# Kernel tuning notes

Hardware: AMD Instinct MI355X
Metric: run time of the kernel (lower is better)

Reference implementation:

```python
import jax, jax.numpy as jnp
import numpy as np

B, S, D, H = 2, 2048, 1024, 16
HD = D // H
DFF = 4 * D
EPS = 1e-5


def layernorm(x, g, b):
    mu = jnp.mean(x, axis=-1, keepdims=True)
    var = jnp.mean((x - mu) ** 2, axis=-1, keepdims=True)
    return (x - mu) * jax.lax.rsqrt(var + EPS) * g + b


def setup_inputs() -> dict:
    key = jax.random.key(0)
    ks = jax.random.split(key, 16)
    sc = 0.02
    return {
        "x": jax.random.normal(ks[0], (B, S, D), jnp.float32),
        "pos_emb": jax.random.normal(ks[1], (S, D), jnp.float32),
        "ln1_g": jnp.ones((D,), jnp.float32),
        "ln1_b": jnp.zeros((D,), jnp.float32),
        "w_qkv": jax.random.normal(ks[2], (D, 3 * D), jnp.float32) * sc,
        "b_qkv": jnp.zeros((3 * D,), jnp.float32),
        "w_o": jax.random.normal(ks[3], (D, D), jnp.float32) * sc,
        "b_o": jnp.zeros((D,), jnp.float32),
        "ln2_g": jnp.ones((D,), jnp.float32),
        "ln2_b": jnp.zeros((D,), jnp.float32),
        "w_fc": jax.random.normal(ks[4], (D, DFF), jnp.float32) * sc,
        "b_fc": jnp.zeros((DFF,), jnp.float32),
        "w_proj": jax.random.normal(ks[5], (DFF, D), jnp.float32) * sc,
        "b_proj": jnp.zeros((D,), jnp.float32),
    }


def reference(x, pos_emb, ln1_g, ln1_b, w_qkv, b_qkv, w_o, b_o,
              ln2_g, ln2_b, w_fc, b_fc, w_proj, b_proj):
    # --- attention sub-block: x + attn(norm1(x) + pos_emb) ---
    h = layernorm(x, ln1_g, ln1_b) + pos_emb  # [B,S,D]
    qkv = h @ w_qkv + b_qkv                    # [B,S,3D]
    qkv = qkv.reshape(B, S, 3, H, HD).transpose(2, 0, 3, 1, 4)  # [3,B,H,S,HD]
    q, k, v = qkv[0], qkv[1], qkv[2]
    # naive full attention: materialize [B,H,S,S]
    w = jnp.einsum('bhqd,bhkd->bhqk', q, k) / jnp.sqrt(jnp.float32(HD))
    causal = jnp.tril(jnp.ones((S, S), bool))  # True = keep
    w = jnp.where(causal, w, -jnp.inf)
    a = jax.nn.softmax(w, axis=-1)
    out = jnp.einsum('bhqk,bhkd->bhqd', a, v)   # [B,H,S,HD]
    out = out.transpose(0, 2, 1, 3).reshape(B, S, D)
    x = x + out @ w_o + b_o
    # --- MLP sub-block: x + mlp(norm2(x)) ---
    m = layernorm(x, ln2_g, ln2_b)
    m = jax.nn.gelu(m @ w_fc + b_fc) @ w_proj + b_proj
    return x + m
```

## Files before the change

kernel.cpp:

```cpp
#include <hip/hip_runtime.h>
#include <hip/hip_bf16.h>

typedef __hip_bfloat16 bf16_t;
typedef __bf16 bf16x8 __attribute__((ext_vector_type(8)));
typedef float f32x4 __attribute__((ext_vector_type(4)));

__device__ __forceinline__ void gload_lds16(const void* g, void* l) {
  __builtin_amdgcn_global_load_lds(
      (const __attribute__((address_space(1))) void*)g,
      (__attribute__((address_space(3))) void*)l, 16, 0, 0);
}

__device__ __forceinline__ unsigned short f2bf(float f) {
  bf16_t h = __float2bfloat16(f);
  return reinterpret_cast<unsigned short&>(h);
}

__global__ __launch_bounds__(256) void wtrans_kernel(
    const float* __restrict__ in, bf16_t* __restrict__ out, int K, int N) {
  __shared__ float tile[32][33];
  int tx = threadIdx.x, ty = threadIdx.y;
  int n = blockIdx.x * 32 + tx;
  int k0 = blockIdx.y * 32 + ty;
#pragma unroll
  for (int j = 0; j < 32; j += 8) tile[ty + j][tx] = in[(size_t)(k0 + j) * N + n];
  __syncthreads();
  int k = blockIdx.y * 32 + tx;
  int n0 = blockIdx.x * 32 + ty;
#pragma unroll
  for (int j = 0; j < 32; j += 8)
    out[(size_t)(n0 + j) * K + k] = __float2bfloat16(tile[tx][ty + j]);
}

__global__ __launch_bounds__(256) void ln_kernel(
    const float* __restrict__ x, const float* __restrict__ g,
    const float* __restrict__ b, const float* __restrict__ pos,
    bf16_t* __restrict__ out, int S) {
  int row = blockIdx.x;
  int tid = threadIdx.x;
  const float4* xr = (const float4*)(x + (size_t)row * 1024);
  float4 v = xr[tid];
  float s1 = v.x + v.y + v.z + v.w;
  float s2 = v.x * v.x + v.y * v.y + v.z * v.z + v.w * v.w;
#pragma unroll
  for (int off = 1; off < 64; off <<= 1) {
    s1 += __shfl_xor(s1, off);
    s2 += __shfl_xor(s2, off);
  }
  __shared__ float red[2][4];
  int w = tid >> 6;
  if ((tid & 63) == 0) { red[0][w] = s1; red[1][w] = s2; }
  __syncthreads();
  s1 = red[0][0] + red[0][1] + red[0][2] + red[0][3];
  s2 = red[1][0] + red[1][1] + red[1][2] + red[1][3];
  float mu = s1 * (1.f / 1024.f);
  float var = s2 * (1.f / 1024.f) - mu * mu;
  float rs = rsqrtf(var + 1e-5f);
  float4 gg = ((const float4*)g)[tid];
  float4 bb = ((const float4*)b)[tid];
  float4 pp = {0.f, 0.f, 0.f, 0.f};
  if (pos) pp = ((const float4*)(pos + (size_t)(row & (S - 1)) * 1024))[tid];
  ushort4 o4;
  o4.x = f2bf((v.x - mu) * rs * gg.x + bb.x + pp.x);
  o4.y = f2bf((v.y - mu) * rs * gg.y + bb.y + pp.y);
  o4.z = f2bf((v.z - mu) * rs * gg.z + bb.z + pp.z);
  o4.w = f2bf((v.w - mu) * rs * gg.w + bb.w + pp.w);
  ((ushort4*)(out + (size_t)row * 1024))[tid] = o4;
}

template <int EPI>
__global__ __launch_bounds__(256) void gemm_bt(
    const bf16_t* __restrict__ A, const bf16_t* __restrict__ BT,
    const float* __restrict__ bias, const float* __restrict__ resid,
    float* __restrict__ outf, bf16_t* __restrict__ outb,
    bf16_t* __restrict__ qb, bf16_t* __restrict__ kb, bf16_t* __restrict__ vb,
    int M, int N, int K) {
  __shared__ char lds[32768];
  char* As = lds;
  char* Bs = lds + 16384;
  int tid = threadIdx.x;
  int l = tid & 63;
  int w = tid >> 6;
  int wr = w >> 1, wc = w & 1;
  int ll = l & 15, lg = l >> 4;
  int rowBase = blockIdx.y * 128, colBase = blockIdx.x * 128;

  f32x4 acc[4][4];
  f32x4 z = {0.f, 0.f, 0.f, 0.f};
#pragma unroll
  for (int i = 0; i < 4; i++)
#pragma unroll
    for (int j = 0; j < 4; j++) acc[i][j] = z;

  int nkt = K >> 6;
  for (int kt = 0; kt < nkt; ++kt) {
    __syncthreads();
#pragma unroll
    for (int i = 0; i < 4; i++) {
      int p = i * 4096 + tid * 16;
      int o = p ^ (((p >> 7) & 7) << 4);
      int r = o >> 7, c = (o & 127) >> 1;
      gload_lds16(A + (size_t)(rowBase + r) * K + kt * 64 + c, As + p);
    }
#pragma unroll
    for (int i = 0; i < 4; i++) {
      int p = i * 4096 + tid * 16;
      int o = p ^ (((p >> 7) & 7) << 4);
      int r = o >> 7, c = (o & 127) >> 1;
      gload_lds16(BT + (size_t)(colBase + r) * K + kt * 64 + c, Bs + p);
    }
    __syncthreads();

    bf16x8 af[4][2], bfv[4][2];
#pragma unroll
    for (int mi = 0; mi < 4; mi++) {
      int row = wr * 64 + mi * 16 + ll;
#pragma unroll
      for (int kk = 0; kk < 2; kk++) {
        int o = (row << 7) + (kk << 6) + (lg << 4);
        af[mi][kk] = *(const bf16x8*)(As + (o ^ ((row & 7) << 4)));
      }
    }
#pragma unroll
    for (int ni = 0; ni < 4; ni++) {
      int row = wc * 64 + ni * 16 + ll;
#pragma unroll
      for (int kk = 0; kk < 2; kk++) {
        int o = (row << 7) + (kk << 6) + (lg << 4);
        bfv[ni][kk] = *(const bf16x8*)(Bs + (o ^ ((row & 7) << 4)));
      }
    }
#pragma unroll
    for (int mi = 0; mi < 4; mi++)
#pragma unroll
      for (int ni = 0; ni < 4; ni++)
#pragma unroll
        for (int kk = 0; kk < 2; kk++)
          acc[mi][ni] = __builtin_amdgcn_mfma_f32_16x16x32_bf16(
              af[mi][kk], bfv[ni][kk], acc[mi][ni], 0, 0, 0);
  }

#pragma unroll
  for (int mi = 0; mi < 4; mi++) {
#pragma unroll
    for (int ni = 0; ni < 4; ni++) {
#pragma unroll
      for (int j = 0; j < 4; j++) {
        int grow = rowBase + wr * 64 + mi * 16 + lg * 4 + j;
        int gcol = colBase + wc * 64 + ni * 16 + ll;
        float v = acc[mi][ni][j] + bias[gcol];
        if (EPI == 0) {
          int bb = grow >> 11, s = grow & 2047;
          int t = gcol >> 10, rem = gcol & 1023;
          int h = rem >> 6, d = rem & 63;
          size_t bh = (size_t)(bb * 16 + h);
          if (t == 0)
            qb[(bh * 2048 + s) * 64 + d] = __float2bfloat16(v);
          else if (t == 1)
            kb[(bh * 2048 + s) * 64 + d] = __float2bfloat16(v);
          else
            vb[(bh * 64 + d) * 2048 + s] = __float2bfloat16(v);
        } else if (EPI == 1) {
          size_t idx = (size_t)grow * N + gcol;
          outf[idx] = resid[idx] + v;
        } else {
          float c3 = v * v * v;
          float t = tanhf(0.7978845608028654f * (v + 0.044715f * c3));
          outb[(size_t)grow * N + gcol] = __float2bfloat16(0.5f * v * (1.f + t));
        }
      }
    }
  }
}

__global__ __launch_bounds__(256, 2) void attn_kernel(
    const bf16_t* __restrict__ qb, const bf16_t* __restrict__ kb,
    const bf16_t* __restrict__ vbT, bf16_t* __restrict__ op, int S) {
  int id = blockIdx.x;
  int bh = id & 31;
  int qt = 15 - (id >> 5);
  int tid = threadIdx.x;
  int w = tid >> 6, l = tid & 63;
  int ll = l & 15, lg = l >> 4;
  __shared__ char lds[49152];
  char* Pw = lds + 32768 + w * 4096;

  int qbase = qt * 128;
  int qlo = qbase + w * 32;
  int qhi = qlo + 31;

  bf16x8 qf[2][2];
#pragma unroll
  for (int mi = 0; mi < 2; mi++) {
    const bf16_t* qrp = qb + ((size_t)bh * S + qbase + w * 32 + mi * 16 + ll) * 64;
#pragma unroll
    for (int kk = 0; kk < 2; kk++) qf[mi][kk] = *(const bf16x8*)(qrp + kk * 32 + lg * 8);
  }

  f32x4 Oacc[2][4];
  f32x4 z = {0.f, 0.f, 0.f, 0.f};
#pragma unroll
  for (int mi = 0; mi < 2; mi++)
#pragma unroll
    for (int i = 0; i < 4; i++) Oacc[mi][i] = z;
  float mrow[2][4], lrow[2][4];
#pragma unroll
  for (int mi = 0; mi < 2; mi++)
#pragma unroll
    for (int j = 0; j < 4; j++) { mrow[mi][j] = -INFINITY; lrow[mi][j] = 0.f; }

  int last = 2 * qt + 1;

  auto STAGE = [&](int kt, int c) {
    char* Kt = lds + c * 8192;
    char* Vt = lds + 16384 + c * 8192;
#pragma unroll
    for (int i = 0; i < 2; ++i) {
      int p = i * 4096 + tid * 16;
      int o = p ^ (((p >> 7) & 7) << 4);
      int r = o >> 7, cc = (o & 127) >> 1;
      gload_lds16(kb + ((size_t)bh * S + kt * 64 + r) * 64 + cc, Kt + p);
    }
#pragma unroll
    for (int i = 0; i < 2; ++i) {
      int p = i * 4096 + tid * 16;
      int o = p ^ (((p >> 7) & 7) << 4);
      int d = o >> 7, cc = (o & 127) >> 1;
      gload_lds16(vbT + ((size_t)bh * 64 + d) * S + kt * 64 + cc, Vt + p);
    }
  };

  STAGE(0, 0);
  int c = 0;
  for (int kt = 0; kt <= last; ++kt) {
    __builtin_amdgcn_s_barrier();
    if (kt < last) {
      STAGE(kt + 1, c ^ 1);
      asm volatile("s_waitcnt vmcnt(4)" ::: "memory");
    } else {
      asm volatile("s_waitcnt vmcnt(0)" ::: "memory");
    }
    __builtin_amdgcn_s_barrier();
    asm volatile("" ::: "memory");

    if (kt * 64 <= qhi) {
      char* Kt = lds + c * 8192;
      char* Vt = lds + 16384 + c * 8192;

      bf16x8 kf[4][2];
#pragma unroll
      for (int f = 0; f < 4; f++) {
        int row = f * 16 + ll;
#pragma unroll
        for (int kk = 0; kk < 2; kk++) {
          int o = (row << 7) + (kk << 6) + (lg << 4);
          kf[f][kk] = *(const bf16x8*)(Kt + (o ^ ((row & 7) << 4)));
        }
      }
      f32x4 sfr[2][4];
#pragma unroll
      for (int mi = 0; mi < 2; mi++)
#pragma unroll
        for (int f = 0; f < 4; f++) {
          sfr[mi][f] = z;
#pragma unroll
          for (int kk = 0; kk < 2; kk++)
            sfr[mi][f] = __builtin_amdgcn_mfma_f32_16x16x32_bf16(
                qf[mi][kk], kf[f][kk], sfr[mi][f], 0, 0, 0);
        }

      bool diag = (kt * 64 + 63) > qlo;
#pragma unroll
      for (int mi = 0; mi < 2; mi++) {
#pragma unroll
        for (int j = 0; j < 4; j++) {
          int qr = qlo + mi * 16 + lg * 4 + j;
          float mx = -INFINITY;
#pragma unroll
          for (int f = 0; f < 4; f++) {
            float s = sfr[mi][f][j] * 0.125f;
            if (diag && (kt * 64 + f * 16 + ll) > qr) s = -INFINITY;
            sfr[mi][f][j] = s;
            mx = fmaxf(mx, s);
          }
#pragma unroll
          for (int off = 1; off < 16; off <<= 1) mx = fmaxf(mx, __shfl_xor(mx, off));
          float mnew = fmaxf(mrow[mi][j], mx);
          float fj = __expf(mrow[mi][j] - mnew);
          float sum = 0.f;
#pragma unroll
          for (int f = 0; f < 4; f++) {
            float p = __expf(sfr[mi][f][j] - mnew);
            sfr[mi][f][j] = p;
            sum += p;
          }
#pragma unroll
          for (int off = 1; off < 16; off <<= 1) sum += __shfl_xor(sum, off);
          lrow[mi][j] = lrow[mi][j] * fj + sum;
          mrow[mi][j] = mnew;
#pragma unroll
          for (int fd = 0; fd < 4; fd++) Oacc[mi][fd][j] *= fj;
        }
      }

#pragma unroll
      for (int mi = 0; mi < 2; mi++)
#pragma unroll
        for (int j = 0; j < 4; j++) {
          int r = mi * 16 + lg * 4 + j;
#pragma unroll
          for (int f = 0; f < 4; f++) {
            int o = (r << 7) + ((f * 16 + ll) << 1);
            *(unsigned short*)(Pw + (o ^ ((r & 7) << 4))) = f2bf(sfr[mi][f][j]);
          }
        }

      bf16x8 vf2[4][2];
#pragma unroll
      for (int fd = 0; fd < 4; fd++) {
        int row = fd * 16 + ll;
#pragma unroll
        for (int kk = 0; kk < 2; kk++) {
          int o = (row << 7) + (kk << 6) + (lg << 4);
          vf2[fd][kk] = *(const bf16x8*)(Vt + (o ^ ((row & 7) << 4)));
        }
      }
      bf16x8 pf[2][2];
#pragma unroll
      for (int mi = 0; mi < 2; mi++) {
        int pr = mi * 16 + ll;
#pragma unroll
        for (int kk = 0; kk < 2; kk++) {
          int o = (pr << 7) + (kk << 6) + (lg << 4);
          pf[mi][kk] = *(const bf16x8*)(Pw + (o ^ ((pr & 7) << 4)));
        }
      }
#pragma unroll
      for (int mi = 0; mi < 2; mi++)
#pragma unroll
        for (int fd = 0; fd < 4; fd++)
#pragma unroll
          for (int kk = 0; kk < 2; kk++)
            Oacc[mi][fd] = __builtin_amdgcn_mfma_f32_16x16x32_bf16(
                pf[mi][kk], vf2[fd][kk], Oacc[mi][fd], 0, 0, 0);
    }
    c ^= 1;
  }

  int b = bh >> 4, hh = bh & 15;
#pragma unroll
  for (int mi = 0; mi < 2; mi++)
#pragma unroll
    for (int j = 0; j < 4; j++) {
      int srow = qbase + w * 32 + mi * 16 + lg * 4 + j;
      float inv = 1.f / lrow[mi][j];
#pragma unroll
      for (int fd = 0; fd < 4; fd++) {
        int col = (hh << 6) + (fd << 4) + ll;
        op[((size_t)b * S + srow) * 1024 + col] = __float2bfloat16(Oacc[mi][fd][j] * inv);
      }
    }
}

extern "C" void kernel_launch(void* const* d_in, const int* in_sizes, int n_in,
                              void* d_out, int out_size, void* d_ws, size_t ws_size,
                              hipStream_t stream) {
  const float* x = (const float*)d_in[0];
  const float* pos_emb = (const float*)d_in[1];
  const float* ln1_g = (const float*)d_in[2];
  const float* ln1_b = (const float*)d_in[3];
  const float* w_qkv = (const float*)d_in[4];
  const float* b_qkv = (const float*)d_in[5];
  const float* w_o = (const float*)d_in[6];
  const float* b_o = (const float*)d_in[7];
  const float* ln2_g = (const float*)d_in[8];
  const float* ln2_b = (const float*)d_in[9];
  const float* w_fc = (const float*)d_in[10];
  const float* b_fc = (const float*)d_in[11];
  const float* w_proj = (const float*)d_in[12];
  const float* b_proj = (const float*)d_in[13];

  char* ws = (char*)d_ws;
  auto take = [&](size_t bytes) {
    char* p = ws;
    ws += (bytes + 255) & ~(size_t)255;
    return p;
  };
  bf16_t* wqkvT = (bf16_t*)take(3072ull * 1024 * 2);
  bf16_t* woT = (bf16_t*)take(1024ull * 1024 * 2);
  bf16_t* wfcT = (bf16_t*)take(4096ull * 1024 * 2);
  bf16_t* wprojT = (bf16_t*)take(1024ull * 4096 * 2);
  bf16_t* h = (bf16_t*)take(4096ull * 1024 * 2);
  bf16_t* qbuf = (bf16_t*)take(32ull * 2048 * 64 * 2);
  bf16_t* kbuf = (bf16_t*)take(32ull * 2048 * 64 * 2);
  bf16_t* vbuf = (bf16_t*)take(32ull * 2048 * 64 * 2);
  bf16_t* aout = (bf16_t*)take(4096ull * 1024 * 2);
  float* x2 = (float*)take(4096ull * 1024 * 4);
  bf16_t* mb = (bf16_t*)take(4096ull * 1024 * 2);
  bf16_t* fca = (bf16_t*)qbuf;

  dim3 tb(32, 8);
  wtrans_kernel<<<dim3(3072 / 32, 1024 / 32), tb, 0, stream>>>(w_qkv, wqkvT, 1024, 3072);
  wtrans_kernel<<<dim3(1024 / 32, 1024 / 32), tb, 0, stream>>>(w_o, woT, 1024, 1024);
  wtrans_kernel<<<dim3(4096 / 32, 1024 / 32), tb, 0, stream>>>(w_fc, wfcT, 1024, 4096);
  wtrans_kernel<<<dim3(1024 / 32, 4096 / 32), tb, 0, stream>>>(w_proj, wprojT, 4096, 1024);

  ln_kernel<<<4096, 256, 0, stream>>>(x, ln1_g, ln1_b, pos_emb, h, 2048);

  gemm_bt<0><<<dim3(24, 32), 256, 0, stream>>>(h, wqkvT, b_qkv, nullptr, nullptr,
                                               nullptr, qbuf, kbuf, vbuf, 4096, 3072, 1024);

  attn_kernel<<<dim3(512), 256, 0, stream>>>(qbuf, kbuf, vbuf, aout, 2048);

  gemm_bt<1><<<dim3(8, 32), 256, 0, stream>>>(aout, woT, b_o, x, x2, nullptr,
                                              nullptr, nullptr, nullptr, 4096, 1024, 1024);

  ln_kernel<<<4096, 256, 0, stream>>>(x2, ln2_g, ln2_b, nullptr, mb, 2048);

  gemm_bt<2><<<dim3(32, 32), 256, 0, stream>>>(mb, wfcT, b_fc, nullptr, nullptr,
                                               fca, nullptr, nullptr, nullptr, 4096, 4096, 1024);

  gemm_bt<1><<<dim3(8, 32), 256, 0, stream>>>(fca, wprojT, b_proj, x2, (float*)d_out,
                                              nullptr, nullptr, nullptr, nullptr, 4096, 1024, 4096);
}
```

Measured before the change: 452.2 us.

## Double-buffer LDS tiles in small-grid GEMMs to overlap loads with MFMA

Adds a DBUF template flag to the bf16 GEMM. When it is set, the kernel uses two 32KB LDS stages and prefetches the next K tile with global_load_lds while computing on the current one, using vmcnt waits and raw barriers. It is enabled only for the two 256-block GEMMs (output projection and MLP down-projection), where low occupancy leaves load latency exposed. In exchange, LDS per block doubles to 64KB, which can lower occupancy, and the hand-written vmcnt counting is fragile.

```diff
diff --git a/kernel.cpp b/kernel.cpp
--- a/kernel.cpp
+++ b/kernel.cpp
@@ -68,16 +68,14 @@
   ((ushort4*)(out + (size_t)row * 1024))[tid] = o4;
 }
 
-template <int EPI>
+template <int EPI, int DBUF>
 __global__ __launch_bounds__(256) void gemm_bt(
     const bf16_t* __restrict__ A, const bf16_t* __restrict__ BT,
     const float* __restrict__ bias, const float* __restrict__ resid,
     float* __restrict__ outf, bf16_t* __restrict__ outb,
     bf16_t* __restrict__ qb, bf16_t* __restrict__ kb, bf16_t* __restrict__ vb,
     int M, int N, int K) {
-  __shared__ char lds[32768];
-  char* As = lds;
-  char* Bs = lds + 16384;
+  __shared__ char lds[DBUF ? 65536 : 32768];
   int tid = threadIdx.x;
   int l = tid & 63;
   int w = tid >> 6;
@@ -92,24 +90,45 @@
 #pragma unroll
     for (int j = 0; j < 4; j++) acc[i][j] = z;
 
-  int nkt = K >> 6;
-  for (int kt = 0; kt < nkt; ++kt) {
-    __syncthreads();
+  auto STAGE = [&](int kt, int c) {
 #pragma unroll
     for (int i = 0; i < 4; i++) {
       int p = i * 4096 + tid * 16;
       int o = p ^ (((p >> 7) & 7) << 4);
-      int r = o >> 7, c = (o & 127) >> 1;
-      gload_lds16(A + (size_t)(rowBase + r) * K + kt * 64 + c, As + p);
+      int r = o >> 7, cc = (o & 127) >> 1;
+      gload_lds16(A + (size_t)(rowBase + r) * K + kt * 64 + cc, lds + c * 32768 + p);
     }
 #pragma unroll
     for (int i = 0; i < 4; i++) {
       int p = i * 4096 + tid * 16;
       int o = p ^ (((p >> 7) & 7) << 4);
-      int r = o >> 7, c = (o & 127) >> 1;
-      gload_lds16(BT + (size_t)(colBase + r) * K + kt * 64 + c, Bs + p);
-    }
-    __syncthreads();
+      int r = o >> 7, cc = (o & 127) >> 1;
+      gload_lds16(BT + (size_t)(colBase + r) * K + kt * 64 + cc,
+                  lds + c * 32768 + 16384 + p);
+    }
+  };
+
+  int nkt = K >> 6;
+  if (DBUF) STAGE(0, 0);
+  int cbuf = 0;
+  for (int kt = 0; kt < nkt; ++kt) {
+    if (DBUF) {
+      __builtin_amdgcn_s_barrier();
+      if (kt + 1 < nkt) {
+        STAGE(kt + 1, cbuf ^ 1);
+        asm volatile("s_waitcnt vmcnt(8)" ::: "memory");
+      } else {
+        asm volatile("s_waitcnt vmcnt(0)" ::: "memory");
+      }
+      __builtin_amdgcn_s_barrier();
+      asm volatile("" ::: "memory");
+    } else {
+      __syncthreads();
+      STAGE(kt, 0);
+      __syncthreads();
+    }
+    char* Ab = lds + cbuf * 32768;
+    char* Bb = Ab + 16384;
 
     bf16x8 af[4][2], bfv[4][2];
 #pragma unroll
@@ -118,7 +137,7 @@
 #pragma unroll
       for (int kk = 0; kk < 2; kk++) {
         int o = (row << 7) + (kk << 6) + (lg << 4);
-        af[mi][kk] = *(const bf16x8*)(As + (o ^ ((row & 7) << 4)));
+        af[mi][kk] = *(const bf16x8*)(Ab + (o ^ ((row & 7) << 4)));
       }
     }
 #pragma unroll
@@ -127,7 +146,7 @@
 #pragma unroll
       for (int kk = 0; kk < 2; kk++) {
         int o = (row << 7) + (kk << 6) + (lg << 4);
-        bfv[ni][kk] = *(const bf16x8*)(Bs + (o ^ ((row & 7) << 4)));
+        bfv[ni][kk] = *(const bf16x8*)(Bb + (o ^ ((row & 7) << 4)));
       }
     }
 #pragma unroll
@@ -138,6 +157,7 @@
         for (int kk = 0; kk < 2; kk++)
           acc[mi][ni] = __builtin_amdgcn_mfma_f32_16x16x32_bf16(
               af[mi][kk], bfv[ni][kk], acc[mi][ni], 0, 0, 0);
+    if (DBUF) cbuf ^= 1;
   }
 
 #pragma unroll
@@ -407,19 +427,19 @@
 
   ln_kernel<<<4096, 256, 0, stream>>>(x, ln1_g, ln1_b, pos_emb, h, 2048);
 
-  gemm_bt<0><<<dim3(24, 32), 256, 0, stream>>>(h, wqkvT, b_qkv, nullptr, nullptr,
-                                               nullptr, qbuf, kbuf, vbuf, 4096, 3072, 1024);
+  gemm_bt<0, 0><<<dim3(24, 32), 256, 0, stream>>>(h, wqkvT, b_qkv, nullptr, nullptr,
+                                                  nullptr, qbuf, kbuf, vbuf, 4096, 3072, 1024);
 
   attn_kernel<<<dim3(512), 256, 0, stream>>>(qbuf, kbuf, vbuf, aout, 2048);
 
-  gemm_bt<1><<<dim3(8, 32), 256, 0, stream>>>(aout, woT, b_o, x, x2, nullptr,
-                                              nullptr, nullptr, nullptr, 4096, 1024, 1024);
+  gemm_bt<1, 1><<<dim3(8, 32), 256, 0, stream>>>(aout, woT, b_o, x, x2, nullptr,
+                                                 nullptr, nullptr, nullptr, 4096, 1024, 1024);
 
   ln_kernel<<<4096, 256, 0, stream>>>(x2, ln2_g, ln2_b, nullptr, mb, 2048);
 
-  gemm_bt<2><<<dim3(32, 32), 256, 0, stream>>>(mb, wfcT, b_fc, nullptr, nullptr,
-                                               fca, nullptr, nullptr, nullptr, 4096, 4096, 1024);
-
-  gemm_bt<1><<<dim3(8, 32), 256, 0, stream>>>(fca, wprojT, b_proj, x2, (float*)d_out,
-                                              nullptr, nullptr, nullptr, nullptr, 4096, 1024, 4096);
-}
+  gemm_bt<2, 0><<<dim3(32, 32), 256, 0, stream>>>(mb, wfcT, b_fc, nullptr, nullptr,
+                                                  fca, nullptr, nullptr, nullptr, 4096, 4096, 1024);
+
+  gemm_bt<1, 1><<<dim3(8, 32), 256, 0, stream>>>(fca, wprojT, b_proj, x2, (float*)d_out,
+                                                 nullptr, nullptr, nullptr, nullptr, 4096, 1024, 4096);
+}
```

Result: faster. 417.2 us (-7.7%).
